# Kernel tuning notes

Measured on AMD Instinct MI355X. Metric: run time of the kernel, lower is better.

Reference implementation:

```python
import jax, jax.numpy as jnp
import numpy as np
import math

DIM = 1280
NUM_HEADS = 16
HEAD_DIM = DIM // NUM_HEADS  # 80
SEQ = 3072


def setup_inputs() -> dict:
    key = jax.random.key(0)
    ks = jax.random.split(key, 6)
    hidden_states = jax.random.normal(ks[0], (SEQ, DIM), dtype=jnp.float32)
    cu_seqlens = jnp.array([0, 768, 1536, 2304, 3072], dtype=jnp.int32)
    # rotary angles for half the head dim, as produced by the vision rotary embedding
    rotary_pos_emb = jax.random.uniform(ks[1], (SEQ, HEAD_DIM // 2), dtype=jnp.float32) * 10.0
    qkv_w = jax.random.normal(ks[2], (3 * DIM, DIM), dtype=jnp.float32) * (1.0 / math.sqrt(DIM))
    qkv_b = jax.random.normal(ks[3], (3 * DIM,), dtype=jnp.float32) * 0.02
    proj_w = jax.random.normal(ks[4], (DIM, DIM), dtype=jnp.float32) * (1.0 / math.sqrt(DIM))
    proj_b = jax.random.normal(ks[5], (DIM,), dtype=jnp.float32) * 0.02
    return {"hidden_states": hidden_states, "cu_seqlens": cu_seqlens,
            "rotary_pos_emb": rotary_pos_emb, "qkv_w": qkv_w, "qkv_b": qkv_b,
            "proj_w": proj_w, "proj_b": proj_b}


def _rotate_half(x):
    half = x.shape[-1] // 2
    return jnp.concatenate([-x[..., half:], x[..., :half]], axis=-1)


def _apply_rotary(t, rotary_pos_emb):
    # t: [seq, heads, head_dim]; rotary_pos_emb: [seq, head_dim//2]
    emb = jnp.concatenate([rotary_pos_emb, rotary_pos_emb], axis=-1)  # [seq, head_dim]
    cos = jnp.cos(emb)[:, None, :]
    sin = jnp.sin(emb)[:, None, :]
    return t * cos + _rotate_half(t) * sin


def reference(hidden_states, cu_seqlens, rotary_pos_emb, qkv_w, qkv_b, proj_w, proj_b):
    seq = hidden_states.shape[0]
    qkv = hidden_states @ qkv_w.T + qkv_b                       # [seq, 3*dim]
    qkv = qkv.reshape(seq, 3, NUM_HEADS, HEAD_DIM)
    q, k, v = qkv[:, 0], qkv[:, 1], qkv[:, 2]                   # [seq, h, d]
    q = _apply_rotary(q, rotary_pos_emb)
    k = _apply_rotary(k, rotary_pos_emb)

    # block-diagonal mask: token i attends to token j iff same segment
    seg = jnp.searchsorted(cu_seqlens[1:], jnp.arange(seq), side='right')
    same = seg[:, None] == seg[None, :]                         # [seq, seq] bool
    neg = jnp.finfo(q.dtype).min
    add_mask = jnp.where(same, jnp.float32(0), neg).astype(q.dtype)

    scale = 1.0 / math.sqrt(HEAD_DIM)
    scores = jnp.einsum('nhd,mhd->hnm', q, k) * scale           # [h, seq, seq]
    scores = scores + add_mask[None, :, :]
    attn = jax.nn.softmax(scores.astype(jnp.float32), axis=-1).astype(q.dtype)
    out = jnp.einsum('hnm,mhd->nhd', attn, v).reshape(seq, DIM)
    return out @ proj_w.T + proj_b
```

## Files before the change

kernel.cpp:

```cpp
#include <hip/hip_runtime.h>

#define SEQ 3072
#define NH 16
#define HD 80
#define SEGLEN 768

typedef unsigned short u16;
typedef unsigned int u32;
typedef float f32x4 __attribute__((ext_vector_type(4)));
typedef __bf16 bf16x8 __attribute__((ext_vector_type(8)));
typedef short short8 __attribute__((ext_vector_type(8)));
typedef u16 u16x4 __attribute__((ext_vector_type(4)));

#define WAITV(N) asm volatile("s_waitcnt vmcnt(" #N ")" ::: "memory")

__device__ __forceinline__ u16 f2bf(float f) {
  u32 u = __builtin_bit_cast(u32, f);
  u32 r = u + 0x7fffu + ((u >> 16) & 1u);
  return (u16)(r >> 16);
}
__device__ __forceinline__ float bf2f(u16 x) {
  u32 u = ((u32)x) << 16;
  return __builtin_bit_cast(float, u);
}

__device__ __forceinline__ f32x4 mfma16(short8 a, short8 b, f32x4 c) {
  return __builtin_amdgcn_mfma_f32_16x16x32_bf16(
      __builtin_bit_cast(bf16x8, a), __builtin_bit_cast(bf16x8, b), c, 0, 0, 0);
}

__device__ __forceinline__ void gload_lds16(const u16* g, u16* l) {
  __builtin_amdgcn_global_load_lds(
      (const __attribute__((address_space(1))) u32*)(g),
      (__attribute__((address_space(3))) u32*)(l), 16, 0, 0);
}

__global__ __launch_bounds__(256) void cvt3(const float* __restrict__ a, u16* __restrict__ ao, int na,
                                            const float* __restrict__ b, u16* __restrict__ bo, int nb,
                                            const float* __restrict__ c, u16* __restrict__ co, int nc) {
  int i = blockIdx.x * 256 + threadIdx.x;
  const float* src;
  u16* dst;
  int n;
  if (i < na) { src = a; dst = ao; n = i; }
  else if (i < na + nb) { src = b; dst = bo; n = i - na; }
  else if (i < na + nb + nc) { src = c; dst = co; n = i - na - nb; }
  else return;
  f32x4 v = ((const f32x4*)src)[n];
  u16x4 o;
  o[0] = f2bf(v[0]); o[1] = f2bf(v[1]); o[2] = f2bf(v[2]); o[3] = f2bf(v[3]);
  ((u16x4*)dst)[n] = o;
}

template <int OUT_BF16>
__global__ __launch_bounds__(256) void gemm_p4(
    const u16* __restrict__ A, const u16* __restrict__ B,
    const float* __restrict__ bias, void* __restrict__ Cv,
    int M, int N, int K) {
  __shared__ u16 LB[4][8192];
  const int tid = threadIdx.x, lane = tid & 63, w = tid >> 6;
  const int wr = (w >> 1) * 64, wc = (w & 1) * 64;
  const int lr = lane & 15, lg = lane >> 4;
  const int br = blockIdx.y * 128, bc = blockIdx.x * 128;
  const int NT = K >> 5;

  f32x4 acc[4][4];
#pragma unroll
  for (int m = 0; m < 4; ++m)
#pragma unroll
    for (int n = 0; n < 4; ++n) acc[m][n] = (f32x4){0.f, 0.f, 0.f, 0.f};

  const int r0 = tid >> 2, s0 = tid & 3;
  const int scol = ((s0 - (r0 >> 1)) & 3) << 3;
  const u16* aptr0 = A + (br + r0) * K + scol;
  const u16* aptr1 = A + (br + r0 + 64) * K + scol;
  const u16* bptr0 = B + (bc + r0) * K + scol;
  const u16* bptr1 = B + (bc + r0 + 64) * K + scol;

  auto stage = [&](int t, int buf) {
    const int k0 = t * 32;
    gload_lds16(aptr0 + k0, &LB[buf][tid * 8]);
    gload_lds16(aptr1 + k0, &LB[buf][(tid + 256) * 8]);
    gload_lds16(bptr0 + k0, &LB[buf][4096 + tid * 8]);
    gload_lds16(bptr1 + k0, &LB[buf][4096 + (tid + 256) * 8]);
  };

  int aoff[4], boff[4];
#pragma unroll
  for (int m = 0; m < 4; ++m) {
    int row = wr + m * 16 + lr;
    aoff[m] = row * 64 + ((lg + (row >> 1)) & 3) * 16;
  }
#pragma unroll
  for (int n = 0; n < 4; ++n) {
    int row = wc + n * 16 + lr;
    boff[n] = 8192 + row * 64 + ((lg + (row >> 1)) & 3) * 16;
  }

  auto dostep = [&](int t, int buf, bool issue, int wn) {
    if (issue) stage(t + 3, (t + 3) & 3);
    const char* base = (const char*)&LB[buf][0];
    short8 af[4], bf[4];
#pragma unroll
    for (int m = 0; m < 4; ++m) af[m] = *(const short8*)(base + aoff[m]);
#pragma unroll
    for (int n = 0; n < 4; ++n) bf[n] = *(const short8*)(base + boff[n]);
    __builtin_amdgcn_s_setprio(1);
#pragma unroll
    for (int m = 0; m < 4; ++m)
#pragma unroll
      for (int n = 0; n < 4; ++n) acc[m][n] = mfma16(af[m], bf[n], acc[m][n]);
    __builtin_amdgcn_s_setprio(0);
    if (wn == 8) WAITV(8);
    else if (wn == 4) WAITV(4);
    else if (wn == 0) WAITV(0);
    if (wn >= 0) __builtin_amdgcn_s_barrier();
  };

  stage(0, 0);
  stage(1, 1);
  stage(2, 2);
  WAITV(8);
  __builtin_amdgcn_s_barrier();

  int t = 0;
  for (; t < NT - 4; t += 4) {
    dostep(t + 0, 0, true, 8);
    dostep(t + 1, 1, true, 8);
    dostep(t + 2, 2, true, 8);
    dostep(t + 3, 3, true, 8);
  }
  dostep(NT - 4, 0, true, 8);
  dostep(NT - 3, 1, false, 4);
  dostep(NT - 2, 2, false, 0);
  dostep(NT - 1, 3, false, -1);

#pragma unroll
  for (int n = 0; n < 4; ++n) {
    int col = bc + wc + n * 16 + lr;
    float bv = bias[col];
#pragma unroll
    for (int m = 0; m < 4; ++m) {
      int rowb = br + wr + m * 16 + lg * 4;
#pragma unroll
      for (int r = 0; r < 4; ++r) {
        float v = acc[m][n][r] + bv;
        if (OUT_BF16)
          ((u16*)Cv)[(rowb + r) * N + col] = f2bf(v);
        else
          ((float*)Cv)[(rowb + r) * N + col] = v;
      }
    }
  }
}

__global__ __launch_bounds__(256) void rope_qk(
    const u16* __restrict__ qkvb, const float* __restrict__ rpe,
    u16* __restrict__ qb, u16* __restrict__ kb) {
  const float QSCL = 0.16129841769519493f;
  int i = blockIdx.x;
  const u16* row = qkvb + i * 3840;
#pragma unroll
  for (int it = 0; it < 5; ++it) {
    int idx = it * 256 + threadIdx.x;
    int d = idx % 80;
    float e = rpe[i * 40 + (d % 40)];
    float s, c;
    sincosf(e, &s, &c);
    float qv = bf2f(row[idx]);
    float qo = (d < 40) ? -bf2f(row[idx + 40]) : bf2f(row[idx - 40]);
    float kv = bf2f(row[1280 + idx]);
    float ko = (d < 40) ? -bf2f(row[1280 + idx + 40]) : bf2f(row[1280 + idx - 40]);
    int o = i * 1280 + idx;
    qb[o] = f2bf((qv * c + qo * s) * QSCL);
    kb[o] = f2bf(kv * c + ko * s);
  }
}

__global__ __launch_bounds__(256) void vtrans(const u16* __restrict__ qkvb,
                                              u16* __restrict__ vt) {
  __shared__ u16 tile[64 * 84];
  const int tid = threadIdx.x;
  const int h = blockIdx.y, s0 = blockIdx.x * 64;
#pragma unroll
  for (int c = 0; c < 20; ++c) {
    int ch = c * 256 + tid;
    int r = ch / 80, d = ch % 80;
    tile[r * 84 + d] = qkvb[(s0 + r) * 3840 + 2560 + h * 80 + d];
  }
  __syncthreads();
#pragma unroll
  for (int c = 0; c < 20; ++c) {
    int ch = c * 256 + tid;
    int d = ch >> 6, r = ch & 63;
    vt[(h * 96 + d) * 3072 + s0 + r] = tile[r * 84 + d];
  }
  if (tid < 64) vt[(h * 96 + 80) * 3072 + s0 + tid] = 0x3F80;
}

__global__ __launch_bounds__(256) void attn_kern(
    const u16* __restrict__ qb, const u16* __restrict__ kb,
    const u16* __restrict__ vt, u16* __restrict__ ob) {
  __shared__ u16 SH[26176];
  char* shb = (char*)SH;
  const int tid = threadIdx.x, lane = tid & 63, w = tid >> 6;
  const int lr = lane & 15, lg = lane >> 4;
  const int xcd = blockIdx.x & 7, t = blockIdx.x >> 3;
  const int qt = t % 12, shhi = t / 12;
  const int sh = xcd + shhi * 8;
  const int seg = sh >> 4, h = sh & 15;
  const int qrow = seg * SEGLEN + qt * 64 + w * 16 + lr;

  short8 qf[3];
#pragma unroll
  for (int kk = 0; kk < 3; ++kk) {
    int d = kk * 32 + lg * 8;
    if (d < 80)
      qf[kk] = *(const short8*)(qb + qrow * 1280 + h * 80 + d);
    else
      qf[kk] = (short8){0, 0, 0, 0, 0, 0, 0, 0};
  }
  f32x4 oa[6];
#pragma unroll
  for (int n = 0; n < 6; ++n) oa[n] = (f32x4){0.f, 0.f, 0.f, 0.f};
  float mrow[4] = {-1e30f, -1e30f, -1e30f, -1e30f};

  const u16* kseg = kb + seg * SEGLEN * 1280 + h * 80;
  const u16* vseg = vt + (h * 96) * 3072 + seg * SEGLEN;

  auto stageK = [&](int buf, int it) {
    const u16* kbase = kseg + it * 64 * 1280;
#pragma unroll
    for (int c = 0; c < 4; ++c) {
      int ch = c * 256 + tid;
      int kv = ch >> 4, sl = ch & 15;
      gload_lds16(kbase + kv * 1280 + ((sl ^ (kv & 7)) << 3),
                  (u16*)(shb + buf * 16384 + ch * 16));
    }
  };
  auto stageV = [&](int it) {
    const u16* vbase = vseg + it * 64;
#pragma unroll
    for (int c = 0; c < 3; ++c) {
      int ch = c * 256 + tid;
      if (ch < 648) {
        int d = ch >> 3, sl = ch & 7;
        gload_lds16(vbase + d * 3072 + ((sl ^ (d & 7)) << 3),
                    (u16*)(shb + 32768 + ch * 16));
      }
    }
  };

  stageK(0, 0);
  stageV(0);
  __syncthreads();
  int cur = 0;
  char* PsW = shb + 43136 + w * 2304;
  const char* Vc = shb + 32768;

  for (int it = 0; it < 12; ++it) {
    if (it > 0) stageV(it);
    if (it < 11) stageK(cur ^ 1, it + 1);
    const char* Kc = shb + cur * 16384;
    f32x4 sf[4];
#pragma unroll
    for (int n = 0; n < 4; ++n) {
      sf[n] = (f32x4){0.f, 0.f, 0.f, 0.f};
#pragma unroll
      for (int kk = 0; kk < 3; ++kk) {
        int row = n * 16 + lr;
        int X = kk * 64 + lg * 16;
        short8 kf = *(const short8*)(Kc + row * 256 + (X ^ ((row & 7) << 4)));
        __builtin_amdgcn_s_setprio(1);
        sf[n] = mfma16(qf[kk], kf, sf[n]);
        __builtin_amdgcn_s_setprio(0);
      }
    }
#pragma unroll
    for (int r = 0; r < 4; ++r) {
      float s0 = sf[0][r], s1 = sf[1][r], s2 = sf[2][r], s3 = sf[3][r];
      float mx = fmaxf(fmaxf(s0, s1), fmaxf(s2, s3));
      mx = fmaxf(mx, __shfl_xor(mx, 1, 16));
      mx = fmaxf(mx, __shfl_xor(mx, 2, 16));
      mx = fmaxf(mx, __shfl_xor(mx, 4, 16));
      mx = fmaxf(mx, __shfl_xor(mx, 8, 16));
      float m = fmaxf(mrow[r], mx);
      float f = exp2f(mrow[r] - m);
      mrow[r] = m;
      float p0 = exp2f(s0 - m), p1 = exp2f(s1 - m);
      float p2 = exp2f(s2 - m), p3 = exp2f(s3 - m);
#pragma unroll
      for (int n = 0; n < 6; ++n) oa[n][r] *= f;
      int offb = (lg * 4 + r) * 144 + lr * 2;
      *(u16*)(PsW + offb + ((lg ^ 0) << 5)) = f2bf(p0);
      *(u16*)(PsW + offb + ((lg ^ 1) << 5)) = f2bf(p1);
      *(u16*)(PsW + offb + ((lg ^ 2) << 5)) = f2bf(p2);
      *(u16*)(PsW + offb + ((lg ^ 3) << 5)) = f2bf(p3);
    }
    __syncthreads();
#pragma unroll
    for (int kt = 0; kt < 2; ++kt) {
      short8 pf = *(const short8*)(PsW + lr * 144 +
                                   ((((kt << 1) + (lg >> 1)) ^ (lr >> 2)) << 5) +
                                   ((lg & 1) << 4));
#pragma unroll
      for (int n = 0; n < 6; ++n) {
        int dcol = n * 16 + lr;
        int X = kt * 64 + lg * 16;
        short8 vf = *(const short8*)(Vc + dcol * 128 + (X ^ ((dcol & 7) << 4)));
        __builtin_amdgcn_s_setprio(1);
        oa[n] = mfma16(pf, vf, oa[n]);
        __builtin_amdgcn_s_setprio(0);
      }
    }
    __syncthreads();
    cur ^= 1;
  }
#pragma unroll
  for (int r = 0; r < 4; ++r) {
    float lsum = __shfl(oa[5][r], lane & 48, 64);
    float linv = 1.0f / lsum;
    int orow = seg * SEGLEN + qt * 64 + w * 16 + lg * 4 + r;
#pragma unroll
    for (int n = 0; n < 5; ++n)
      ob[orow * 1280 + h * 80 + n * 16 + lr] = f2bf(oa[n][r] * linv);
  }
}

extern "C" void kernel_launch(void* const* d_in, const int* in_sizes, int n_in,
                              void* d_out, int out_size, void* d_ws, size_t ws_size,
                              hipStream_t stream) {
  const float* hs = (const float*)d_in[0];
  const float* rpe = (const float*)d_in[2];
  const float* qkvw = (const float*)d_in[3];
  const float* qkv_b = (const float*)d_in[4];
  const float* pw = (const float*)d_in[5];
  const float* pb = (const float*)d_in[6];
  float* out = (float*)d_out;

  char* ws = (char*)d_ws;
  u16* hsb = (u16*)(ws);
  u16* wqkvb = (u16*)(ws + 7864320);
  u16* wprojb = (u16*)(ws + 17694720);
  u16* qkvb = (u16*)(ws + 20971520);
  u16* vt = (u16*)(ws + 44564480);
  u16* qb = hsb;
  u16* kb = wqkvb;
  u16* aob = qkvb;

  cvt3<<<10240, 256, 0, stream>>>(hs, hsb, 983040, qkvw, wqkvb, 1228800, pw, wprojb, 409600);
  gemm_p4<1><<<dim3(30, 24), 256, 0, stream>>>(hsb, wqkvb, qkv_b, qkvb, 3072, 3840, 1280);
  rope_qk<<<3072, 256, 0, stream>>>(qkvb, rpe, qb, kb);
  vtrans<<<dim3(48, 16), 256, 0, stream>>>(qkvb, vt);
  attn_kern<<<768, 256, 0, stream>>>(qb, kb, vt, aob);
  gemm_p4<0><<<dim3(10, 24), 256, 0, stream>>>(aob, wprojb, pb, out, 3072, 1280, 1280);
}
```

Before: 141.1 us.

## Template GEMM tiles, use 3-stage pipeline, XCD-aware block swizzle, and fuse rope/vtrans

The GEMM is generalized over per-warp tile counts and now uses a 3-buffer LDS pipeline instead of 4. Block indices are remapped so neighbouring tiles land on the same XCD. The output projection switches to 64x128 tiles, doubling its grid from 240 to 480 blocks to fill the CUs better. The rope and V-transpose kernels are merged into one launch to save a launch and a tail. In exchange the shallower prefetch may hide less load latency, and the smaller projection tiles reuse each loaded operand less.

```diff
diff --git a/kernel.cpp b/kernel.cpp
--- a/kernel.cpp
+++ b/kernel.cpp
@@ -52,95 +52,102 @@
   ((u16x4*)dst)[n] = o;
 }
 
-template <int OUT_BF16>
-__global__ __launch_bounds__(256) void gemm_p4(
+template <int OUT_BF16, int WM, int WN>
+__global__ __launch_bounds__(256) void gemm_p3(
     const u16* __restrict__ A, const u16* __restrict__ B,
     const float* __restrict__ bias, void* __restrict__ Cv,
     int M, int N, int K) {
-  __shared__ u16 LB[4][8192];
+  constexpr int BM = 32 * WM, BN = 32 * WN;
+  constexpr int ROWS = BM + BN;
+  constexpr int L = ROWS / 64;
+  __shared__ u16 LB[3][ROWS * 32];
   const int tid = threadIdx.x, lane = tid & 63, w = tid >> 6;
-  const int wr = (w >> 1) * 64, wc = (w & 1) * 64;
+  const int wr = (w >> 1) * (WM * 16), wc = (w & 1) * (WN * 16);
   const int lr = lane & 15, lg = lane >> 4;
-  const int br = blockIdx.y * 128, bc = blockIdx.x * 128;
+  const int gx = gridDim.x;
+  const int flat = blockIdx.y * gx + blockIdx.x;
+  const int cpx = (gx * gridDim.y) >> 3;
+  const int f = (flat & 7) * cpx + (flat >> 3);
+  const int bx = f % gx, by = f / gx;
+  const int br = by * BM, bc = bx * BN;
   const int NT = K >> 5;
 
-  f32x4 acc[4][4];
-#pragma unroll
-  for (int m = 0; m < 4; ++m)
-#pragma unroll
-    for (int n = 0; n < 4; ++n) acc[m][n] = (f32x4){0.f, 0.f, 0.f, 0.f};
-
-  const int r0 = tid >> 2, s0 = tid & 3;
-  const int scol = ((s0 - (r0 >> 1)) & 3) << 3;
-  const u16* aptr0 = A + (br + r0) * K + scol;
-  const u16* aptr1 = A + (br + r0 + 64) * K + scol;
-  const u16* bptr0 = B + (bc + r0) * K + scol;
-  const u16* bptr1 = B + (bc + r0 + 64) * K + scol;
-
+  f32x4 acc[WM][WN];
+#pragma unroll
+  for (int m = 0; m < WM; ++m)
+#pragma unroll
+    for (int n = 0; n < WN; ++n) acc[m][n] = (f32x4){0.f, 0.f, 0.f, 0.f};
+
+  const u16* sp[L];
+#pragma unroll
+  for (int c = 0; c < L; ++c) {
+    int ch = c * 256 + tid;
+    int row = ch >> 2, sl = ch & 3;
+    int scol = ((sl - (row >> 1)) & 3) << 3;
+    sp[c] = (row < BM ? A + (br + row) * (size_t)K
+                      : B + (bc + row - BM) * (size_t)K) + scol;
+  }
   auto stage = [&](int t, int buf) {
-    const int k0 = t * 32;
-    gload_lds16(aptr0 + k0, &LB[buf][tid * 8]);
-    gload_lds16(aptr1 + k0, &LB[buf][(tid + 256) * 8]);
-    gload_lds16(bptr0 + k0, &LB[buf][4096 + tid * 8]);
-    gload_lds16(bptr1 + k0, &LB[buf][4096 + (tid + 256) * 8]);
+#pragma unroll
+    for (int c = 0; c < L; ++c)
+      gload_lds16(sp[c] + t * 32, &LB[buf][(c * 256 + tid) * 8]);
   };
 
-  int aoff[4], boff[4];
-#pragma unroll
-  for (int m = 0; m < 4; ++m) {
+  int aoff[WM], boff[WN];
+#pragma unroll
+  for (int m = 0; m < WM; ++m) {
     int row = wr + m * 16 + lr;
     aoff[m] = row * 64 + ((lg + (row >> 1)) & 3) * 16;
   }
 #pragma unroll
-  for (int n = 0; n < 4; ++n) {
-    int row = wc + n * 16 + lr;
-    boff[n] = 8192 + row * 64 + ((lg + (row >> 1)) & 3) * 16;
-  }
-
-  auto dostep = [&](int t, int buf, bool issue, int wn) {
-    if (issue) stage(t + 3, (t + 3) & 3);
+  for (int n = 0; n < WN; ++n) {
+    int row = BM + wc + n * 16 + lr;
+    boff[n] = row * 64 + ((lg + (row >> 1)) & 3) * 16;
+  }
+
+  auto step = [&](int t, int buf, bool issue, int wn) {
+    if (issue) stage(t + 2, (t + 2) % 3);
     const char* base = (const char*)&LB[buf][0];
-    short8 af[4], bf[4];
-#pragma unroll
-    for (int m = 0; m < 4; ++m) af[m] = *(const short8*)(base + aoff[m]);
-#pragma unroll
-    for (int n = 0; n < 4; ++n) bf[n] = *(const short8*)(base + boff[n]);
+    short8 af[WM], bf[WN];
+#pragma unroll
+    for (int m = 0; m < WM; ++m) af[m] = *(const short8*)(base + aoff[m]);
+#pragma unroll
+    for (int n = 0; n < WN; ++n) bf[n] = *(const short8*)(base + boff[n]);
     __builtin_amdgcn_s_setprio(1);
 #pragma unroll
-    for (int m = 0; m < 4; ++m)
-#pragma unroll
-      for (int n = 0; n < 4; ++n) acc[m][n] = mfma16(af[m], bf[n], acc[m][n]);
+    for (int m = 0; m < WM; ++m)
+#pragma unroll
+      for (int n = 0; n < WN; ++n) acc[m][n] = mfma16(af[m], bf[n], acc[m][n]);
     __builtin_amdgcn_s_setprio(0);
-    if (wn == 8) WAITV(8);
-    else if (wn == 4) WAITV(4);
+    if (wn == 4) WAITV(4);
+    else if (wn == 3) WAITV(3);
     else if (wn == 0) WAITV(0);
     if (wn >= 0) __builtin_amdgcn_s_barrier();
   };
 
   stage(0, 0);
   stage(1, 1);
-  stage(2, 2);
-  WAITV(8);
+  if constexpr (L == 4) WAITV(4);
+  else WAITV(3);
   __builtin_amdgcn_s_barrier();
 
   int t = 0;
-  for (; t < NT - 4; t += 4) {
-    dostep(t + 0, 0, true, 8);
-    dostep(t + 1, 1, true, 8);
-    dostep(t + 2, 2, true, 8);
-    dostep(t + 3, 3, true, 8);
-  }
-  dostep(NT - 4, 0, true, 8);
-  dostep(NT - 3, 1, false, 4);
-  dostep(NT - 2, 2, false, 0);
-  dostep(NT - 1, 3, false, -1);
-
-#pragma unroll
-  for (int n = 0; n < 4; ++n) {
+  for (; t + 3 <= NT - 2; t += 3) {
+    step(t + 0, 0, true, L);
+    step(t + 1, 1, true, L);
+    step(t + 2, 2, true, L);
+  }
+  step(NT - 4, 0, true, L);
+  step(NT - 3, 1, true, L);
+  step(NT - 2, 2, false, 0);
+  step(NT - 1, 0, false, -1);
+
+#pragma unroll
+  for (int n = 0; n < WN; ++n) {
     int col = bc + wc + n * 16 + lr;
     float bv = bias[col];
 #pragma unroll
-    for (int m = 0; m < 4; ++m) {
+    for (int m = 0; m < WM; ++m) {
       int rowb = br + wr + m * 16 + lg * 4;
 #pragma unroll
       for (int r = 0; r < 4; ++r) {
@@ -154,48 +161,47 @@
   }
 }
 
-__global__ __launch_bounds__(256) void rope_qk(
+__global__ __launch_bounds__(256) void prep_kern(
     const u16* __restrict__ qkvb, const float* __restrict__ rpe,
-    u16* __restrict__ qb, u16* __restrict__ kb) {
-  const float QSCL = 0.16129841769519493f;
-  int i = blockIdx.x;
-  const u16* row = qkvb + i * 3840;
-#pragma unroll
-  for (int it = 0; it < 5; ++it) {
-    int idx = it * 256 + threadIdx.x;
-    int d = idx % 80;
-    float e = rpe[i * 40 + (d % 40)];
-    float s, c;
-    sincosf(e, &s, &c);
-    float qv = bf2f(row[idx]);
-    float qo = (d < 40) ? -bf2f(row[idx + 40]) : bf2f(row[idx - 40]);
-    float kv = bf2f(row[1280 + idx]);
-    float ko = (d < 40) ? -bf2f(row[1280 + idx + 40]) : bf2f(row[1280 + idx - 40]);
-    int o = i * 1280 + idx;
-    qb[o] = f2bf((qv * c + qo * s) * QSCL);
-    kb[o] = f2bf(kv * c + ko * s);
-  }
-}
-
-__global__ __launch_bounds__(256) void vtrans(const u16* __restrict__ qkvb,
-                                              u16* __restrict__ vt) {
-  __shared__ u16 tile[64 * 84];
-  const int tid = threadIdx.x;
-  const int h = blockIdx.y, s0 = blockIdx.x * 64;
-#pragma unroll
-  for (int c = 0; c < 20; ++c) {
-    int ch = c * 256 + tid;
-    int r = ch / 80, d = ch % 80;
-    tile[r * 84 + d] = qkvb[(s0 + r) * 3840 + 2560 + h * 80 + d];
-  }
-  __syncthreads();
-#pragma unroll
-  for (int c = 0; c < 20; ++c) {
-    int ch = c * 256 + tid;
-    int d = ch >> 6, r = ch & 63;
-    vt[(h * 96 + d) * 3072 + s0 + r] = tile[r * 84 + d];
-  }
-  if (tid < 64) vt[(h * 96 + 80) * 3072 + s0 + tid] = 0x3F80;
+    u16* __restrict__ qb, u16* __restrict__ kb, u16* __restrict__ vt) {
+  const int bid = blockIdx.x, tid = threadIdx.x;
+  if (bid < 3072) {
+    const float QSCL = 0.16129841769519493f;
+    const u16* row = qkvb + bid * 3840;
+#pragma unroll
+    for (int it = 0; it < 5; ++it) {
+      int idx = it * 256 + tid;
+      int d = idx % 80;
+      float e = rpe[bid * 40 + (d % 40)];
+      float s, c;
+      sincosf(e, &s, &c);
+      float qv = bf2f(row[idx]);
+      float qo = (d < 40) ? -bf2f(row[idx + 40]) : bf2f(row[idx - 40]);
+      float kv = bf2f(row[1280 + idx]);
+      float ko = (d < 40) ? -bf2f(row[1280 + idx + 40]) : bf2f(row[1280 + idx - 40]);
+      int o = bid * 1280 + idx;
+      qb[o] = f2bf((qv * c + qo * s) * QSCL);
+      kb[o] = f2bf(kv * c + ko * s);
+    }
+  } else {
+    __shared__ u16 tile[64 * 84];
+    const int vb = bid - 3072;
+    const int s0 = (vb % 48) * 64, h = vb / 48;
+#pragma unroll
+    for (int c = 0; c < 20; ++c) {
+      int ch = c * 256 + tid;
+      int r = ch / 80, d = ch % 80;
+      tile[r * 84 + d] = qkvb[(s0 + r) * 3840 + 2560 + h * 80 + d];
+    }
+    __syncthreads();
+#pragma unroll
+    for (int c = 0; c < 20; ++c) {
+      int ch = c * 256 + tid;
+      int d = ch >> 6, r = ch & 63;
+      vt[(h * 96 + d) * 3072 + s0 + r] = tile[r * 84 + d];
+    }
+    if (tid < 64) vt[(h * 96 + 80) * 3072 + s0 + tid] = 0x3F80;
+  }
 }
 
 __global__ __launch_bounds__(256) void attn_kern(
@@ -349,9 +355,8 @@
   u16* aob = qkvb;
 
   cvt3<<<10240, 256, 0, stream>>>(hs, hsb, 983040, qkvw, wqkvb, 1228800, pw, wprojb, 409600);
-  gemm_p4<1><<<dim3(30, 24), 256, 0, stream>>>(hsb, wqkvb, qkv_b, qkvb, 3072, 3840, 1280);
-  rope_qk<<<3072, 256, 0, stream>>>(qkvb, rpe, qb, kb);
-  vtrans<<<dim3(48, 16), 256, 0, stream>>>(qkvb, vt);
+  gemm_p3<1, 4, 4><<<dim3(30, 24), 256, 0, stream>>>(hsb, wqkvb, qkv_b, qkvb, 3072, 3840, 1280);
+  prep_kern<<<3840, 256, 0, stream>>>(qkvb, rpe, qb, kb, vt);
   attn_kern<<<768, 256, 0, stream>>>(qb, kb, vt, aob);
-  gemm_p4<0><<<dim3(10, 24), 256, 0, stream>>>(aob, wprojb, pb, out, 3072, 1280, 1280);
-}
+  gemm_p3<0, 2, 4><<<dim3(10, 48), 256, 0, stream>>>(aob, wprojb, pb, out, 3072, 1280, 1280);
+}
```

Result: faster. 137.8 us (-2.4%).
